# Kernel optimization log

Measured on AMD Instinct MI355X. Metric: run time of the kernel, lower is better.

## Reference

```python
import jax, jax.numpy as jnp
import numpy as np

E = 8
DIMS = [512, 1024, 1024, 512]
BATCH = 2048


def _init_w(key, shape):
    a = np.sqrt(6.0 / (shape[-2] * shape[-1]))
    return jax.random.uniform(key, shape, dtype=jnp.float32, minval=-a, maxval=a)


def setup_inputs() -> dict:
    key = jax.random.key(0)
    ks = jax.random.split(key, 8)
    inp = {
        "weight_blend": jax.random.uniform(ks[0], (BATCH, E), dtype=jnp.float32),
        "x": jax.random.normal(ks[1], (BATCH, DIMS[0]), dtype=jnp.float32),
    }
    for i in range(3):
        inp[f"W{i}"] = _init_w(ks[2 + i], (E, DIMS[i + 1], DIMS[i]))
        inp[f"B{i}"] = jnp.zeros((E, DIMS[i + 1], 1), dtype=jnp.float32)
    return inp


def reference(weight_blend, x, W0, B0, W1, B1, W2, B2):
    Ws = [W0, W1, W2]
    Bs = [B0, B1, B2]
    acts = [jax.nn.elu, jax.nn.elu, None]
    for W, B, act in zip(Ws, Bs, acts):
        # dropout p=0 -> identity
        # blended-expert GEMM: sum_e wb[b,e] * (W[e] @ x[b]) == einsum
        t = jnp.einsum("be,eoi,bi->bo", weight_blend, W, x)
        bias = jnp.einsum("be,eo->bo", weight_blend, B[..., 0])
        x = t + bias
        if act is not None:
            x = act(x)
    return x
```

## Files before the change

kernel.cpp:

```cpp
#include <hip/hip_runtime.h>
#include <math.h>

typedef __attribute__((ext_vector_type(8))) short bf16x8;
typedef __attribute__((ext_vector_type(4))) float f32x4;

#define NEXP 8
#define BATCH 2048

__device__ __forceinline__ unsigned short f2bf(float f) {
    union { float f; unsigned u; } v; v.f = f;
    unsigned r = v.u + 0x7FFFu + ((v.u >> 16) & 1u);
    return (unsigned short)(r >> 16);
}

__device__ __forceinline__ float elu_fast(float v) {
    return v > 0.f ? v : (exp2f(v * 1.4426950408889634f) - 1.0f);
}

__device__ __forceinline__ void gl_lds(const char* g, char* l) {
    __builtin_amdgcn_global_load_lds(
        (const __attribute__((address_space(1))) void*)g,
        (__attribute__((address_space(3))) void*)l, 16, 0, 0);
}

__global__ __launch_bounds__(256) void pack_all(
    const float* __restrict__ W0, const float* __restrict__ W1,
    const float* __restrict__ W2, const float* __restrict__ x,
    unsigned short* __restrict__ W0p, unsigned short* __restrict__ W1p,
    unsigned short* __restrict__ W2p, unsigned short* __restrict__ x0p)
{
    __shared__ float T[128 * 36];
    const int bid = blockIdx.x, t = threadIdx.x;

    if (bid < 10240) {
        const float* W; unsigned short* out; int KB, Din, Dout, U, lin;
        if (bid < 2048)      { W = W0; out = W0p; KB = 16; Din = 512;  Dout = 1024; U = 4; lin = bid; }
        else if (bid < 6144) { W = W1; out = W1p; KB = 32; Din = 1024; Dout = 1024; U = 4; lin = bid - 2048; }
        else                 { W = W2; out = W2p; KB = 32; Din = 1024; Dout = 512;  U = 2; lin = bid - 6144; }
        const int e  = lin & 7;
        const int r  = lin >> 3;
        const int kb = r % KB;
        const int nb = r / KB;
        const int N0 = nb * 16 * U;
        const int K0 = kb * 32;
        for (int it = 0; it < U / 2; ++it) {
            const int idx = t + 256 * it;
            const int nl = idx >> 3, k4 = (idx & 7) * 4;
            float4 v = *(const float4*)(W + ((size_t)e * Dout + N0 + nl) * Din + K0 + k4);
            *(float4*)(T + nl * 36 + k4) = v;
        }
        __syncthreads();
        if (t < 64 * U) {
            const int u = t >> 6, l = t & 63;
            const float* p = T + (u * 16 + (l & 15)) * 36 + (l >> 4) * 8;
            bf16x8 h;
            #pragma unroll
            for (int j = 0; j < 8; ++j) h[j] = (short)f2bf(p[j]);
            *(bf16x8*)(out + (size_t)lin * (U * 512) + t * 8) = h;
        }
    } else {
        const int lin = bid - 10240;
        const int kb = lin & 15, mb = lin >> 4;
        for (int it = 0; it < 4; ++it) {
            const int idx = t + 256 * it;
            const int ml = idx >> 3, k4 = (idx & 7) * 4;
            float4 v = *(const float4*)(x + (size_t)(mb * 128 + ml) * 512 + kb * 32 + k4);
            *(float4*)(T + ml * 36 + k4) = v;
        }
        __syncthreads();
        #pragma unroll
        for (int it = 0; it < 2; ++it) {
            const int s = t + 256 * it;
            const int g = s >> 6, l = s & 63;
            const float* p = T + (g * 16 + (l & 15)) * 36 + (l >> 4) * 8;
            bf16x8 h;
            #pragma unroll
            for (int j = 0; j < 8; ++j) h[j] = (short)f2bf(p[j]);
            *(bf16x8*)(x0p + (size_t)lin * 4096 + s * 8) = h;
        }
    }
}

template<int UP>
__device__ __forceinline__ void moe_stage(
    char* smem, int bx, int by,
    const unsigned short* __restrict__ Xp,
    const unsigned short* __restrict__ Wp,
    const float* __restrict__ Bias,
    const float* __restrict__ WBl,
    unsigned short* __restrict__ Yout,
    int KB, int Dout, int KBn)
{
    constexpr int PSTR = 68;
    constexpr unsigned BUFB = 40 * 1024;

    const int tid  = threadIdx.x;
    const int wv   = tid >> 6;
    const int mh   = wv >> 2;
    const int ew   = wv & 3;
    const int l    = tid & 63;
    const int lh   = l >> 4;
    const int ll   = l & 15;
    const int e0   = 2 * ew;
    const int m0   = by * 128 + mh * 64;
    const int n0   = bx * 64;
    const int mb   = by;

    f32x4 acc0[4][4], acc1[4][4];
    #pragma unroll
    for (int t = 0; t < 4; ++t)
        #pragma unroll
        for (int u = 0; u < 4; ++u)
            #pragma unroll
            for (int i = 0; i < 4; ++i) { acc0[t][u][i] = 0.f; acc1[t][u][i] = 0.f; }

    const char* xc = (const char*)Xp;
    const char* wc = (const char*)Wp;
    const int fidbase = wv * 5;
    const char* gp[5]; unsigned kst[5];
    #pragma unroll
    for (int s = 0; s < 5; ++s) {
        const int fid = fidbase + s;
        if (fid < 8) {
            gp[s]  = xc + (unsigned)(mb * KB) * 8192u + (unsigned)fid * 1024u + l * 16u;
            kst[s] = 8192u;
        } else {
            const int idx = fid - 8;
            const int e   = 2 * (idx >> 3) + ((idx >> 2) & 1);
            const int u   = idx & 3;
            const int fn  = bx * 4 + u;
            const int nb  = fn / UP;
            const int uu  = fn % UP;
            gp[s]  = wc + (unsigned)((nb * KB * 8 + e) * UP + uu) * 1024u + l * 16u;
            kst[s] = UP * 8192u;
        }
    }

    auto STAGE = [&](int b, int kk) {
        char* lb = smem + (unsigned)b * BUFB + (unsigned)fidbase * 1024u;
        #pragma unroll
        for (int s = 0; s < 5; ++s)
            gl_lds(gp[s] + (unsigned)kk * kst[s], lb + s * 1024);
    };

    auto COMPUTE = [&](int b) {
        const char* sb = smem + (unsigned)b * BUFB;
        bf16x8 aR[4], b0R[4], b1R[4];
        #pragma unroll
        for (int t = 0; t < 4; ++t)
            aR[t] = *(const bf16x8*)(sb + (mh * 4 + t) * 1024 + l * 16);
        #pragma unroll
        for (int u = 0; u < 4; ++u) {
            b0R[u] = *(const bf16x8*)(sb + (8 + ew * 8 + u) * 1024 + l * 16);
            b1R[u] = *(const bf16x8*)(sb + (8 + ew * 8 + 4 + u) * 1024 + l * 16);
        }
        __builtin_amdgcn_s_setprio(1);
        #pragma unroll
        for (int u = 0; u < 4; ++u)
            #pragma unroll
            for (int t = 0; t < 4; ++t) {
                acc0[t][u] = __builtin_amdgcn_mfma_f32_16x16x32_bf16(aR[t], b0R[u], acc0[t][u], 0, 0, 0);
                acc1[t][u] = __builtin_amdgcn_mfma_f32_16x16x32_bf16(aR[t], b1R[u], acc1[t][u], 0, 0, 0);
            }
        __builtin_amdgcn_s_setprio(0);
    };

    STAGE(0, 0);
    __syncthreads();
    for (int kk = 0; kk < KB; ++kk) {
        if (kk + 1 < KB) STAGE((kk + 1) & 1, kk + 1);
        COMPUTE(kk & 1);
        __syncthreads();
    }

    float* epi = (float*)smem;
    float bi0[4], bi1[4];
    #pragma unroll
    for (int u = 0; u < 4; ++u) {
        const int n = n0 + u * 16 + ll;
        bi0[u] = Bias[(size_t)e0 * Dout + n];
        bi1[u] = Bias[(size_t)(e0 + 1) * Dout + n];
    }
    float2 wbp[4][4];
    #pragma unroll
    for (int t = 0; t < 4; ++t)
        #pragma unroll
        for (int r = 0; r < 4; ++r) {
            const int lm = 16 * t + 4 * lh + r;
            wbp[t][r] = ((const float2*)(WBl + (size_t)(m0 + lm) * NEXP))[ew];
        }

    float* pb = epi + ew * (64 * PSTR);
    #pragma unroll
    for (int h = 0; h < 2; ++h) {
        if (mh == h) {
            #pragma unroll
            for (int t = 0; t < 4; ++t)
                #pragma unroll
                for (int r = 0; r < 4; ++r) {
                    const int lm = 16 * t + 4 * lh + r;
                    #pragma unroll
                    for (int u = 0; u < 4; ++u)
                        pb[lm * PSTR + u * 16 + ll] =
                            wbp[t][r].x * (acc0[t][u][r] + bi0[u]) + wbp[t][r].y * (acc1[t][u][r] + bi1[u]);
                }
        }
        __syncthreads();
        {
            const int kbh = wv >> 2;
            const int g   = wv & 3;
            const int rb  = (g * 16 + ll) * PSTR + kbh * 32 + lh * 8;
            bf16x8 hx;
            #pragma unroll
            for (int j = 0; j < 8; ++j) {
                float v = epi[0 * 64 * PSTR + rb + j]
                        + epi[1 * 64 * PSTR + rb + j]
                        + epi[2 * 64 * PSTR + rb + j]
                        + epi[3 * 64 * PSTR + rb + j];
                v = elu_fast(v);
                hx[j] = (short)f2bf(v);
            }
            unsigned short* dst = Yout +
                ((size_t)(mb * KBn + bx * 2 + kbh) * 8 + h * 4 + g) * 512 + l * 8;
            *(bf16x8*)dst = hx;
        }
        if (h == 0) __syncthreads();
    }
}

__device__ __forceinline__ void moe_stage_l2(
    char* smem, int bx, int by,
    const unsigned short* __restrict__ Xp,
    const unsigned short* __restrict__ Wp,
    const float* __restrict__ Bias,
    const float* __restrict__ WBl,
    float* __restrict__ Yout,
    int KB, int Dout)
{
    constexpr int UP = 2;
    constexpr int PSTR = 36;
    constexpr unsigned BUFB = 20 * 1024;

    const int tid  = threadIdx.x;
    const int ew   = tid >> 6;
    const int l    = tid & 63;
    const int lh   = l >> 4;
    const int ll   = l & 15;
    const int e0   = 2 * ew;
    const int m0   = by * 64;
    const int n0   = bx * 32;
    const int mb   = by >> 1;
    const int half = by & 1;

    f32x4 acc0[4][2], acc1[4][2];
    #pragma unroll
    for (int t = 0; t < 4; ++t)
        #pragma unroll
        for (int u = 0; u < 2; ++u)
            #pragma unroll
            for (int i = 0; i < 4; ++i) { acc0[t][u][i] = 0.f; acc1[t][u][i] = 0.f; }

    const char* xc = (const char*)Xp;
    const char* wc = (const char*)Wp;
    const int fidbase = ew * 5;
    const char* gp[5]; unsigned kst[5];
    #pragma unroll
    for (int s = 0; s < 5; ++s) {
        const int fid = fidbase + s;
        if (fid < 4) {
            gp[s]  = xc + (unsigned)(mb * KB) * 8192u + (unsigned)(half * 4 + fid) * 1024u + l * 16u;
            kst[s] = 8192u;
        } else {
            const int idx = fid - 4;
            const int e   = idx >> 1;
            const int u   = idx & 1;
            const int fn  = bx * 2 + u;
            const int nb  = fn / UP;
            const int uu  = fn % UP;
            gp[s]  = wc + (unsigned)((nb * KB * 8 + e) * UP + uu) * 1024u + l * 16u;
            kst[s] = UP * 8192u;
        }
    }

    auto STAGE = [&](int b, int kk) {
        char* lb = smem + (unsigned)b * BUFB + (unsigned)fidbase * 1024u;
        #pragma unroll
        for (int s = 0; s < 5; ++s)
            gl_lds(gp[s] + (unsigned)kk * kst[s], lb + s * 1024);
    };

    auto COMPUTE = [&](int b) {
        const char* sb = smem + (unsigned)b * BUFB;
        bf16x8 aR[4], b0R[2], b1R[2];
        #pragma unroll
        for (int t = 0; t < 4; ++t)
            aR[t] = *(const bf16x8*)(sb + t * 1024 + l * 16);
        #pragma unroll
        for (int u = 0; u < 2; ++u) {
            b0R[u] = *(const bf16x8*)(sb + (4 + e0 * 2 + u) * 1024 + l * 16);
            b1R[u] = *(const bf16x8*)(sb + (4 + (e0 + 1) * 2 + u) * 1024 + l * 16);
        }
        __builtin_amdgcn_s_setprio(1);
        #pragma unroll
        for (int u = 0; u < 2; ++u)
            #pragma unroll
            for (int t = 0; t < 4; ++t) {
                acc0[t][u] = __builtin_amdgcn_mfma_f32_16x16x32_bf16(aR[t], b0R[u], acc0[t][u], 0, 0, 0);
                acc1[t][u] = __builtin_amdgcn_mfma_f32_16x16x32_bf16(aR[t], b1R[u], acc1[t][u], 0, 0, 0);
            }
        __builtin_amdgcn_s_setprio(0);
    };

    STAGE(0, 0);
    __syncthreads();
    for (int kk = 0; kk < KB; ++kk) {
        if (kk + 1 < KB) STAGE((kk + 1) & 1, kk + 1);
        COMPUTE(kk & 1);
        __syncthreads();
    }

    float* epi = (float*)smem;
    float bi0[2], bi1[2];
    #pragma unroll
    for (int u = 0; u < 2; ++u) {
        const int n = n0 + u * 16 + ll;
        bi0[u] = Bias[(size_t)e0 * Dout + n];
        bi1[u] = Bias[(size_t)(e0 + 1) * Dout + n];
    }
    float2 wbp[4][4];
    #pragma unroll
    for (int t = 0; t < 4; ++t)
        #pragma unroll
        for (int r = 0; r < 4; ++r) {
            const int lm = 16 * t + 4 * lh + r;
            wbp[t][r] = ((const float2*)(WBl + (size_t)(m0 + lm) * NEXP))[ew];
        }

    float* pb = epi + ew * (64 * PSTR);
    #pragma unroll
    for (int t = 0; t < 4; ++t)
        #pragma unroll
        for (int r = 0; r < 4; ++r) {
            const int lm = 16 * t + 4 * lh + r;
            #pragma unroll
            for (int u = 0; u < 2; ++u)
                pb[lm * PSTR + u * 16 + ll] =
                    wbp[t][r].x * (acc0[t][u][r] + bi0[u]) + wbp[t][r].y * (acc1[t][u][r] + bi1[u]);
        }
    __syncthreads();

    #pragma unroll
    for (int it = 0; it < 2; ++it) {
        const int idx = tid + 256 * it;
        const int row = idx >> 3;
        const int c4  = (idx & 7) * 4;
        const int rb  = row * PSTR + c4;
        float4 s  = *(const float4*)(epi + 0 * 64 * PSTR + rb);
        float4 q1 = *(const float4*)(epi + 1 * 64 * PSTR + rb);
        float4 q2 = *(const float4*)(epi + 2 * 64 * PSTR + rb);
        float4 q3 = *(const float4*)(epi + 3 * 64 * PSTR + rb);
        s.x += q1.x + q2.x + q3.x;
        s.y += q1.y + q2.y + q3.y;
        s.z += q1.z + q2.z + q3.z;
        s.w += q1.w + q2.w + q3.w;
        *(float4*)(Yout + (size_t)(m0 + row) * Dout + n0 + c4) = s;
    }
}

__device__ __forceinline__ void swz256(int& bx, int& by) {
    const int bid = blockIdx.x;
    const int xcd = bid & 7;
    const int loc = bid >> 3;
    bx = xcd * 2 + (loc & 1);
    by = loc >> 1;
}
__device__ __forceinline__ void swz_pair(int& bx, int& by) {
    const int bid = blockIdx.x;
    const int xcd = bid & 7;
    const int loc = bid >> 3;
    bx = xcd * 2 + (loc & 1);
    by = loc >> 1;
}

__global__ __launch_bounds__(512, 2) void moe_l0(
    const unsigned short* __restrict__ Xp, const unsigned short* __restrict__ Wp,
    const float* __restrict__ Bias, const float* __restrict__ WBl,
    unsigned short* __restrict__ Yout, int KB, int Dout, int KBn)
{
    __shared__ __align__(16) char smem[2 * 40 * 1024];
    int bx, by; swz256(bx, by);
    moe_stage<4>(smem, bx, by, Xp, Wp, Bias, WBl, Yout, KB, Dout, KBn);
}
__global__ __launch_bounds__(512, 2) void moe_l1(
    const unsigned short* __restrict__ Xp, const unsigned short* __restrict__ Wp,
    const float* __restrict__ Bias, const float* __restrict__ WBl,
    unsigned short* __restrict__ Yout, int KB, int Dout, int KBn)
{
    __shared__ __align__(16) char smem[2 * 40 * 1024];
    int bx, by; swz256(bx, by);
    moe_stage<4>(smem, bx, by, Xp, Wp, Bias, WBl, Yout, KB, Dout, KBn);
}
__global__ __launch_bounds__(256, 2) void moe_l2(
    const unsigned short* __restrict__ Xp, const unsigned short* __restrict__ Wp,
    const float* __restrict__ Bias, const float* __restrict__ WBl,
    float* __restrict__ Yout, int KB, int Dout)
{
    __shared__ __align__(16) char smem[2 * 20 * 1024];
    int bx, by; swz_pair(bx, by);
    moe_stage_l2(smem, bx, by, Xp, Wp, Bias, WBl, Yout, KB, Dout);
}

#define BM 64
#define BNF 64
#define BKF 16
#define PAD 4

__global__ __launch_bounds__(256) void moe_layer_f32(
    const float* __restrict__ X, const float* __restrict__ W,
    const float* __restrict__ Bias, const float* __restrict__ WB,
    float* __restrict__ Y, int Din, int Dout, int act)
{
    __shared__ float As[BKF][BM + PAD];
    __shared__ float Bs[BKF][BNF + PAD];
    const int tid = threadIdx.x;
    const int tm = tid >> 4, tn = tid & 15;
    const int m0 = blockIdx.y * BM, n0 = blockIdx.x * BNF;
    const int lr = tid >> 2, lc = (tid & 3) << 2;
    float acc[4][4] = {};
    const float* xrow  = X  + (size_t)(m0 + lr) * Din;
    const float* wbrow = WB + (size_t)(m0 + lr) * NEXP;
    const float* wrow0 = W  + (size_t)(n0 + lr) * Din;
    for (int e = 0; e < NEXP; ++e) {
        const float wbe = wbrow[e];
        const float* wrow = wrow0 + (size_t)e * Dout * Din;
        for (int k0 = 0; k0 < Din; k0 += BKF) {
            float4 av = *(const float4*)(xrow + k0 + lc);
            float4 bv = *(const float4*)(wrow + k0 + lc);
            __syncthreads();
            As[lc+0][lr] = av.x*wbe; As[lc+1][lr] = av.y*wbe;
            As[lc+2][lr] = av.z*wbe; As[lc+3][lr] = av.w*wbe;
            Bs[lc+0][lr] = bv.x; Bs[lc+1][lr] = bv.y;
            Bs[lc+2][lr] = bv.z; Bs[lc+3][lr] = bv.w;
            __syncthreads();
            #pragma unroll
            for (int k = 0; k < BKF; ++k) {
                float4 a = *(const float4*)&As[k][tm << 2];
                float4 b = *(const float4*)&Bs[k][tn << 2];
                acc[0][0]+=a.x*b.x; acc[0][1]+=a.x*b.y; acc[0][2]+=a.x*b.z; acc[0][3]+=a.x*b.w;
                acc[1][0]+=a.y*b.x; acc[1][1]+=a.y*b.y; acc[1][2]+=a.y*b.z; acc[1][3]+=a.y*b.w;
                acc[2][0]+=a.z*b.x; acc[2][1]+=a.z*b.y; acc[2][2]+=a.z*b.z; acc[2][3]+=a.z*b.w;
                acc[3][0]+=a.w*b.x; acc[3][1]+=a.w*b.y; acc[3][2]+=a.w*b.z; acc[3][3]+=a.w*b.w;
            }
        }
    }
    #pragma unroll
    for (int im = 0; im < 4; ++im) {
        const int m = m0 + (tm << 2) + im;
        const float* wbm = WB + (size_t)m * NEXP;
        float wv[NEXP];
        #pragma unroll
        for (int e = 0; e < NEXP; ++e) wv[e] = wbm[e];
        #pragma unroll
        for (int in = 0; in < 4; ++in) {
            const int n = n0 + (tn << 2) + in;
            float bsum = 0.f;
            #pragma unroll
            for (int e = 0; e < NEXP; ++e) bsum += wv[e] * Bias[(size_t)e * Dout + n];
            float v = acc[im][in] + bsum;
            if (act) v = v > 0.f ? v : expm1f(v);
            acc[im][in] = v;
        }
        float4 o = make_float4(acc[im][0], acc[im][1], acc[im][2], acc[im][3]);
        *(float4*)(Y + (size_t)m * Dout + n0 + (tn << 2)) = o;
    }
}

extern "C" void kernel_launch(void* const* d_in, const int* in_sizes, int n_in,
                              void* d_out, int out_size, void* d_ws, size_t ws_size,
                              hipStream_t stream)
{
    (void)in_sizes; (void)n_in; (void)out_size;
    const float* wb = (const float*)d_in[0];
    const float* x  = (const float*)d_in[1];
    const float* W0 = (const float*)d_in[2];
    const float* B0 = (const float*)d_in[3];
    const float* W1 = (const float*)d_in[4];
    const float* B1 = (const float*)d_in[5];
    const float* W2 = (const float*)d_in[6];
    const float* B2 = (const float*)d_in[7];
    float* out = (float*)d_out;

    const size_t NW0 = (size_t)8*1024*512, NW1 = (size_t)8*1024*1024, NW2 = (size_t)8*512*1024;
    const size_t NX0 = (size_t)BATCH*512, NX1 = (size_t)BATCH*1024;
    const size_t need = (NW0 + NW1 + NW2 + NX0 + 2 * NX1) * 2;

    if (ws_size >= need) {
        unsigned short* W0p = (unsigned short*)d_ws;
        unsigned short* W1p = W0p + NW0;
        unsigned short* W2p = W1p + NW1;
        unsigned short* x0p = W2p + NW2;
        unsigned short* x1p = x0p + NX0;
        unsigned short* x2p = x1p + NX1;
        pack_all<<<10496, 256, 0, stream>>>(W0, W1, W2, x, W0p, W1p, W2p, x0p);
        moe_l0<<<256, 512, 0, stream>>>(x0p, W0p, B0, wb, x1p, 16, 1024, 32);
        moe_l1<<<256, 512, 0, stream>>>(x1p, W1p, B1, wb, x2p, 32, 1024, 32);
        moe_l2<<<512, 256, 0, stream>>>(x2p, W2p, B2, wb, out, 32, 512);
    } else {
        float* x1 = (float*)d_ws;
        float* x2 = x1 + (size_t)BATCH * 1024;
        moe_layer_f32<<<dim3(1024/BNF, BATCH/BM), 256, 0, stream>>>(x,  W0, B0, wb, x1, 512,  1024, 1);
        moe_layer_f32<<<dim3(1024/BNF, BATCH/BM), 256, 0, stream>>>(x1, W1, B1, wb, x2, 1024, 1024, 1);
        moe_layer_f32<<<dim3(512/BNF,  BATCH/BM), 256, 0, stream>>>(x2, W2, B2, wb, out, 1024, 512,  0);
    }
}
```

Measured before the change: 186.7 us.

## Triple-buffer LDS and double-buffer register fragments in layer-1 MoE GEMM

Adds a second pipeline variant for the layer-1 kernel. It prefetches three K-stages into LDS through global_load_lds and ping-pongs register fragments so LDS reads for the next stage overlap the MFMAs of the current one. Explicit waitcnt and barrier calls replace the plain __syncthreads. The goal is to hide global and LDS latency behind matrix math. In exchange, LDS per block rises to 120KB, which likely allows only one block per CU instead of two, and register pressure goes up.

```diff
diff --git a/kernel.cpp b/kernel.cpp
--- a/kernel.cpp
+++ b/kernel.cpp
@@ -81,7 +81,7 @@
     }
 }
 
-template<int UP>
+template<int UP, int PIPE>
 __device__ __forceinline__ void moe_stage(
     char* smem, int bx, int by,
     const unsigned short* __restrict__ Xp,
@@ -143,34 +143,92 @@
             gl_lds(gp[s] + (unsigned)kk * kst[s], lb + s * 1024);
     };
 
-    auto COMPUTE = [&](int b) {
-        const char* sb = smem + (unsigned)b * BUFB;
-        bf16x8 aR[4], b0R[4], b1R[4];
-        #pragma unroll
-        for (int t = 0; t < 4; ++t)
-            aR[t] = *(const bf16x8*)(sb + (mh * 4 + t) * 1024 + l * 16);
-        #pragma unroll
-        for (int u = 0; u < 4; ++u) {
-            b0R[u] = *(const bf16x8*)(sb + (8 + ew * 8 + u) * 1024 + l * 16);
-            b1R[u] = *(const bf16x8*)(sb + (8 + ew * 8 + 4 + u) * 1024 + l * 16);
-        }
-        __builtin_amdgcn_s_setprio(1);
-        #pragma unroll
-        for (int u = 0; u < 4; ++u)
-            #pragma unroll
-            for (int t = 0; t < 4; ++t) {
-                acc0[t][u] = __builtin_amdgcn_mfma_f32_16x16x32_bf16(aR[t], b0R[u], acc0[t][u], 0, 0, 0);
-                acc1[t][u] = __builtin_amdgcn_mfma_f32_16x16x32_bf16(aR[t], b1R[u], acc1[t][u], 0, 0, 0);
+    if constexpr (PIPE == 0) {
+        auto COMPUTE = [&](int b) {
+            const char* sb = smem + (unsigned)b * BUFB;
+            bf16x8 aR[4], b0R[4], b1R[4];
+            #pragma unroll
+            for (int t = 0; t < 4; ++t)
+                aR[t] = *(const bf16x8*)(sb + (mh * 4 + t) * 1024 + l * 16);
+            #pragma unroll
+            for (int u = 0; u < 4; ++u) {
+                b0R[u] = *(const bf16x8*)(sb + (8 + ew * 8 + u) * 1024 + l * 16);
+                b1R[u] = *(const bf16x8*)(sb + (8 + ew * 8 + 4 + u) * 1024 + l * 16);
             }
-        __builtin_amdgcn_s_setprio(0);
-    };
-
-    STAGE(0, 0);
-    __syncthreads();
-    for (int kk = 0; kk < KB; ++kk) {
-        if (kk + 1 < KB) STAGE((kk + 1) & 1, kk + 1);
-        COMPUTE(kk & 1);
+            __builtin_amdgcn_s_setprio(1);
+            #pragma unroll
+            for (int u = 0; u < 4; ++u)
+                #pragma unroll
+                for (int t = 0; t < 4; ++t) {
+                    acc0[t][u] = __builtin_amdgcn_mfma_f32_16x16x32_bf16(aR[t], b0R[u], acc0[t][u], 0, 0, 0);
+                    acc1[t][u] = __builtin_amdgcn_mfma_f32_16x16x32_bf16(aR[t], b1R[u], acc1[t][u], 0, 0, 0);
+                }
+            __builtin_amdgcn_s_setprio(0);
+        };
+        STAGE(0, 0);
         __syncthreads();
+        for (int kk = 0; kk < KB; ++kk) {
+            if (kk + 1 < KB) STAGE((kk + 1) & 1, kk + 1);
+            COMPUTE(kk & 1);
+            __syncthreads();
+        }
+    } else {
+        bf16x8 fA[12], fB[12];
+        auto LOADREG = [&](bf16x8 (&fr)[12], int b) {
+            const char* sb = smem + (unsigned)b * BUFB;
+            #pragma unroll
+            for (int t = 0; t < 4; ++t)
+                fr[t] = *(const bf16x8*)(sb + (mh * 4 + t) * 1024 + l * 16);
+            #pragma unroll
+            for (int u = 0; u < 4; ++u) {
+                fr[4 + u] = *(const bf16x8*)(sb + (8 + ew * 8 + u) * 1024 + l * 16);
+                fr[8 + u] = *(const bf16x8*)(sb + (8 + ew * 8 + 4 + u) * 1024 + l * 16);
+            }
+        };
+        auto MFMAALL = [&](bf16x8 (&fr)[12]) {
+            __builtin_amdgcn_s_setprio(1);
+            #pragma unroll
+            for (int u = 0; u < 4; ++u)
+                #pragma unroll
+                for (int t = 0; t < 4; ++t) {
+                    acc0[t][u] = __builtin_amdgcn_mfma_f32_16x16x32_bf16(fr[t], fr[4 + u], acc0[t][u], 0, 0, 0);
+                    acc1[t][u] = __builtin_amdgcn_mfma_f32_16x16x32_bf16(fr[t], fr[8 + u], acc1[t][u], 0, 0, 0);
+                }
+            __builtin_amdgcn_s_setprio(0);
+        };
+
+        STAGE(0, 0); STAGE(1, 1); STAGE(2, 2);
+        asm volatile("s_waitcnt vmcnt(10)" ::: "memory");
+        __builtin_amdgcn_s_barrier();
+        asm volatile("" ::: "memory");
+        LOADREG(fA, 0);
+        asm volatile("s_waitcnt lgkmcnt(0) vmcnt(5)" ::: "memory");
+        __builtin_amdgcn_s_barrier();
+        asm volatile("" ::: "memory");
+
+        int sstage = 0;
+        int snext  = 1;
+        for (int kk = 0; kk < KB; kk += 2) {
+            if (kk + 3 < KB) STAGE(sstage, kk + 3);
+            if (kk + 1 < KB) LOADREG(fB, snext);
+            MFMAALL(fA);
+            if (kk + 3 < KB) asm volatile("s_waitcnt lgkmcnt(0) vmcnt(5)" ::: "memory");
+            else             asm volatile("s_waitcnt lgkmcnt(0) vmcnt(0)" ::: "memory");
+            __builtin_amdgcn_s_barrier();
+            asm volatile("" ::: "memory");
+            sstage = (sstage == 2) ? 0 : sstage + 1;
+            snext  = (snext  == 2) ? 0 : snext  + 1;
+
+            if (kk + 4 < KB) STAGE(sstage, kk + 4);
+            if (kk + 2 < KB) LOADREG(fA, snext);
+            MFMAALL(fB);
+            if (kk + 4 < KB) asm volatile("s_waitcnt lgkmcnt(0) vmcnt(5)" ::: "memory");
+            else             asm volatile("s_waitcnt lgkmcnt(0) vmcnt(0)" ::: "memory");
+            __builtin_amdgcn_s_barrier();
+            asm volatile("" ::: "memory");
+            sstage = (sstage == 2) ? 0 : sstage + 1;
+            snext  = (snext  == 2) ? 0 : snext  + 1;
+        }
     }
 
     float* epi = (float*)smem;
@@ -389,16 +447,16 @@
 {
     __shared__ __align__(16) char smem[2 * 40 * 1024];
     int bx, by; swz256(bx, by);
-    moe_stage<4>(smem, bx, by, Xp, Wp, Bias, WBl, Yout, KB, Dout, KBn);
+    moe_stage<4, 0>(smem, bx, by, Xp, Wp, Bias, WBl, Yout, KB, Dout, KBn);
 }
 __global__ __launch_bounds__(512, 2) void moe_l1(
     const unsigned short* __restrict__ Xp, const unsigned short* __restrict__ Wp,
     const float* __restrict__ Bias, const float* __restrict__ WBl,
     unsigned short* __restrict__ Yout, int KB, int Dout, int KBn)
 {
-    __shared__ __align__(16) char smem[2 * 40 * 1024];
+    __shared__ __align__(16) char smem[3 * 40 * 1024];
     int bx, by; swz256(bx, by);
-    moe_stage<4>(smem, bx, by, Xp, Wp, Bias, WBl, Yout, KB, Dout, KBn);
+    moe_stage<4, 1>(smem, bx, by, Xp, Wp, Bias, WBl, Yout, KB, Dout, KBn);
 }
 __global__ __launch_bounds__(256, 2) void moe_l2(
     const unsigned short* __restrict__ Xp, const unsigned short* __restrict__ Wp,
```

Measured after the change: 206.2 us. 1.1x slower.

## Overlap next-layer weight packing with current-layer GEMM in the same launch

Applied to the files above, without the earlier changes.

The monolithic pack kernel is split so that only W0 and x are converted up front. W1 conversion is folded into the layer-0 GEMM launch as extra blocks, and W2 conversion into the layer-1 launch, so the memory-bound packing can fill idle CUs alongside the compute-bound GEMM tiles. The cost is that the extra pack blocks use the 512-thread GEMM block shape, with threads idle in the W2 path, and they compete with GEMM blocks for occupancy and bandwidth.

```diff
diff --git a/kernel.cpp b/kernel.cpp
--- a/kernel.cpp
+++ b/kernel.cpp
@@ -23,43 +23,38 @@
         (__attribute__((address_space(3))) void*)l, 16, 0, 0);
 }
 
-__global__ __launch_bounds__(256) void pack_all(
-    const float* __restrict__ W0, const float* __restrict__ W1,
-    const float* __restrict__ W2, const float* __restrict__ x,
-    unsigned short* __restrict__ W0p, unsigned short* __restrict__ W1p,
-    unsigned short* __restrict__ W2p, unsigned short* __restrict__ x0p)
+__global__ __launch_bounds__(256) void pack_a(
+    const float* __restrict__ W0, const float* __restrict__ x,
+    unsigned short* __restrict__ W0p, unsigned short* __restrict__ x0p)
 {
     __shared__ float T[128 * 36];
     const int bid = blockIdx.x, t = threadIdx.x;
 
-    if (bid < 10240) {
-        const float* W; unsigned short* out; int KB, Din, Dout, U, lin;
-        if (bid < 2048)      { W = W0; out = W0p; KB = 16; Din = 512;  Dout = 1024; U = 4; lin = bid; }
-        else if (bid < 6144) { W = W1; out = W1p; KB = 32; Din = 1024; Dout = 1024; U = 4; lin = bid - 2048; }
-        else                 { W = W2; out = W2p; KB = 32; Din = 1024; Dout = 512;  U = 2; lin = bid - 6144; }
+    if (bid < 2048) {
+        const int lin = bid;
         const int e  = lin & 7;
         const int r  = lin >> 3;
-        const int kb = r % KB;
-        const int nb = r / KB;
-        const int N0 = nb * 16 * U;
+        const int kb = r % 16;
+        const int nb = r / 16;
+        const int N0 = nb * 64;
         const int K0 = kb * 32;
-        for (int it = 0; it < U / 2; ++it) {
+        for (int it = 0; it < 2; ++it) {
             const int idx = t + 256 * it;
             const int nl = idx >> 3, k4 = (idx & 7) * 4;
-            float4 v = *(const float4*)(W + ((size_t)e * Dout + N0 + nl) * Din + K0 + k4);
+            float4 v = *(const float4*)(W0 + ((size_t)e * 1024 + N0 + nl) * 512 + K0 + k4);
             *(float4*)(T + nl * 36 + k4) = v;
         }
         __syncthreads();
-        if (t < 64 * U) {
+        {
             const int u = t >> 6, l = t & 63;
             const float* p = T + (u * 16 + (l & 15)) * 36 + (l >> 4) * 8;
             bf16x8 h;
             #pragma unroll
             for (int j = 0; j < 8; ++j) h[j] = (short)f2bf(p[j]);
-            *(bf16x8*)(out + (size_t)lin * (U * 512) + t * 8) = h;
+            *(bf16x8*)(W0p + (size_t)lin * 2048 + t * 8) = h;
         }
     } else {
-        const int lin = bid - 10240;
+        const int lin = bid - 2048;
         const int kb = lin & 15, mb = lin >> 4;
         for (int it = 0; it < 4; ++it) {
             const int idx = t + 256 * it;
@@ -367,8 +362,7 @@
     }
 }
 
-__device__ __forceinline__ void swz256(int& bx, int& by) {
-    const int bid = blockIdx.x;
+__device__ __forceinline__ void swz256b(int bid, int& bx, int& by) {
     const int xcd = bid & 7;
     const int loc = bid >> 3;
     bx = xcd * 2 + (loc & 1);
@@ -382,24 +376,82 @@
     by = loc >> 1;
 }
 
-__global__ __launch_bounds__(512, 2) void moe_l0(
+__global__ __launch_bounds__(512, 2) void moe_l0p(
     const unsigned short* __restrict__ Xp, const unsigned short* __restrict__ Wp,
     const float* __restrict__ Bias, const float* __restrict__ WBl,
-    unsigned short* __restrict__ Yout, int KB, int Dout, int KBn)
+    unsigned short* __restrict__ Yout, int KB, int Dout, int KBn,
+    const float* __restrict__ W1, unsigned short* __restrict__ W1p)
 {
     __shared__ __align__(16) char smem[2 * 40 * 1024];
-    int bx, by; swz256(bx, by);
-    moe_stage<4>(smem, bx, by, Xp, Wp, Bias, WBl, Yout, KB, Dout, KBn);
-}
-__global__ __launch_bounds__(512, 2) void moe_l1(
+    const int bid = blockIdx.x;
+    if (bid < 256) {
+        int bx, by; swz256b(bid, bx, by);
+        moe_stage<4>(smem, bx, by, Xp, Wp, Bias, WBl, Yout, KB, Dout, KBn);
+    } else {
+        float* T = (float*)smem;
+        const int t   = threadIdx.x;
+        const int lin = bid - 256;
+        const int e   = lin & 7;
+        const int r   = lin >> 3;
+        const int kb  = r % 32;
+        const int nb  = r / 32;
+        const int N0  = nb * 64;
+        const int K0  = kb * 32;
+        {
+            const int nl = t >> 3, k4 = (t & 7) * 4;
+            float4 v = *(const float4*)(W1 + ((size_t)e * 1024 + N0 + nl) * 1024 + K0 + k4);
+            *(float4*)(T + nl * 36 + k4) = v;
+        }
+        __syncthreads();
+        if (t < 256) {
+            const int u = t >> 6, l = t & 63;
+            const float* p = T + (u * 16 + (l & 15)) * 36 + (l >> 4) * 8;
+            bf16x8 h;
+            #pragma unroll
+            for (int j = 0; j < 8; ++j) h[j] = (short)f2bf(p[j]);
+            *(bf16x8*)(W1p + (size_t)lin * 2048 + t * 8) = h;
+        }
+    }
+}
+
+__global__ __launch_bounds__(512, 2) void moe_l1p(
     const unsigned short* __restrict__ Xp, const unsigned short* __restrict__ Wp,
     const float* __restrict__ Bias, const float* __restrict__ WBl,
-    unsigned short* __restrict__ Yout, int KB, int Dout, int KBn)
+    unsigned short* __restrict__ Yout, int KB, int Dout, int KBn,
+    const float* __restrict__ W2, unsigned short* __restrict__ W2p)
 {
     __shared__ __align__(16) char smem[2 * 40 * 1024];
-    int bx, by; swz256(bx, by);
-    moe_stage<4>(smem, bx, by, Xp, Wp, Bias, WBl, Yout, KB, Dout, KBn);
-}
+    const int bid = blockIdx.x;
+    if (bid < 256) {
+        int bx, by; swz256b(bid, bx, by);
+        moe_stage<4>(smem, bx, by, Xp, Wp, Bias, WBl, Yout, KB, Dout, KBn);
+    } else {
+        float* T = (float*)smem;
+        const int t   = threadIdx.x;
+        const int lin = bid - 256;
+        const int e   = lin & 7;
+        const int r   = lin >> 3;
+        const int kb  = r % 32;
+        const int nb  = r / 32;
+        const int N0  = nb * 32;
+        const int K0  = kb * 32;
+        if (t < 256) {
+            const int nl = t >> 3, k4 = (t & 7) * 4;
+            float4 v = *(const float4*)(W2 + ((size_t)e * 512 + N0 + nl) * 1024 + K0 + k4);
+            *(float4*)(T + nl * 36 + k4) = v;
+        }
+        __syncthreads();
+        if (t < 128) {
+            const int u = t >> 6, l = t & 63;
+            const float* p = T + (u * 16 + (l & 15)) * 36 + (l >> 4) * 8;
+            bf16x8 h;
+            #pragma unroll
+            for (int j = 0; j < 8; ++j) h[j] = (short)f2bf(p[j]);
+            *(bf16x8*)(W2p + (size_t)lin * 1024 + t * 8) = h;
+        }
+    }
+}
+
 __global__ __launch_bounds__(256, 2) void moe_l2(
     const unsigned short* __restrict__ Xp, const unsigned short* __restrict__ Wp,
     const float* __restrict__ Bias, const float* __restrict__ WBl,
@@ -501,9 +553,9 @@
         unsigned short* x0p = W2p + NW2;
         unsigned short* x1p = x0p + NX0;
         unsigned short* x2p = x1p + NX1;
-        pack_all<<<10496, 256, 0, stream>>>(W0, W1, W2, x, W0p, W1p, W2p, x0p);
-        moe_l0<<<256, 512, 0, stream>>>(x0p, W0p, B0, wb, x1p, 16, 1024, 32);
-        moe_l1<<<256, 512, 0, stream>>>(x1p, W1p, B1, wb, x2p, 32, 1024, 32);
+        pack_a<<<2304, 256, 0, stream>>>(W0, x, W0p, x0p);
+        moe_l0p<<<256 + 4096, 512, 0, stream>>>(x0p, W0p, B0, wb, x1p, 16, 1024, 32, W1, W1p);
+        moe_l1p<<<256 + 4096, 512, 0, stream>>>(x1p, W1p, B1, wb, x2p, 32, 1024, 32, W2, W2p);
         moe_l2<<<512, 256, 0, stream>>>(x2p, W2p, B2, wb, out, 32, 512);
     } else {
         float* x1 = (float*)d_ws;
```

Measured after the change: 211.6 us. 13.4% more time.
